# Performance work log

Measured on AMD Instinct MI355X. Metric: run time of the kernel, lower is better.

Reference implementation:

```python
import jax, jax.numpy as jnp
import numpy as np

N_NODES = 50000
N_EDGES = 640000
IN_CH = 128
OUT_CH = 128


def setup_inputs() -> dict:
    key = jax.random.key(0)
    k1, k2, k3, k4 = jax.random.split(key, 4)
    x = jax.random.normal(k1, (N_NODES, IN_CH), dtype=jnp.float32)
    edge_index = jax.random.randint(k2, (2, N_EDGES), 0, N_NODES, dtype=jnp.int32)
    # nn.Linear params: W [out, in], b [out]
    bound = 1.0 / np.sqrt(IN_CH)
    W = jax.random.uniform(k3, (OUT_CH, IN_CH), minval=-bound, maxval=bound, dtype=jnp.float32)
    b = jax.random.uniform(k4, (OUT_CH,), minval=-bound, maxval=bound, dtype=jnp.float32)
    return {"x": x, "edge_index": edge_index, "W": W, "b": b}


def reference(x, edge_index, W, b):
    row, col = edge_index[0], edge_index[1]
    num_nodes = x.shape[0]
    # degree of each destination node (clamped to >= 1)
    deg = jax.ops.segment_sum(jnp.ones(row.shape[0], dtype=x.dtype), row,
                              num_segments=num_nodes)
    deg = jnp.maximum(deg, 1.0)
    # gather neighbor features and scatter-add into destinations
    agg = jax.ops.segment_sum(x[col], row, num_segments=num_nodes)
    agg = agg / deg[:, None]
    # residual + linear
    return (x + agg) @ W.T + b
```

## Files before the change

kernel.cpp:

```cpp
#include <hip/hip_runtime.h>

#define N_NODES 50000
#define N_EDGES 640000
#define CH 128
#define NBINS 49
#define BINCAP 16384
#define CAPR 48
#define NTILES 782

typedef __bf16 bf16_t;
typedef bf16_t bf16x8 __attribute__((ext_vector_type(8)));
typedef float f32x4 __attribute__((ext_vector_type(4)));

__device__ __forceinline__ ushort f2bf(float f) {
  union { float f; unsigned u; } v; v.f = f;
  unsigned r = v.u + 0x7FFFu + ((v.u >> 16) & 1u);
  return (ushort)(r >> 16);
}
__device__ __forceinline__ float bflo(unsigned u) {
  union { unsigned u; float f; } v; v.u = u << 16; return v.f;
}
__device__ __forceinline__ float bfhi(unsigned u) {
  union { unsigned u; float f; } v; v.u = u & 0xFFFF0000u; return v.f;
}
__device__ __forceinline__ unsigned pack2(float lo, float hi) {
  return (unsigned)f2bf(lo) | ((unsigned)f2bf(hi) << 16);
}


__global__ __launch_bounds__(256) void init(const float4* __restrict__ W4,
                                            uint4* __restrict__ Wb4,
                                            int* __restrict__ bincur) {
  int i = blockIdx.x * 256 + threadIdx.x;
  if (i < NBINS) bincur[i] = 0;
  if (i < 2048) {
    float4 c = W4[i * 2], d = W4[i * 2 + 1];
    uint4 w;
    w.x = pack2(c.x, c.y); w.y = pack2(c.z, c.w);
    w.z = pack2(d.x, d.y); w.w = pack2(d.z, d.w);
    Wb4[i] = w;
  }
}

__global__ __launch_bounds__(256) void fill_conv(const int* __restrict__ row,
                                                 const int* __restrict__ col,
                                                 int* __restrict__ bincur,
                                                 unsigned* __restrict__ binArr,
                                                 const float4* __restrict__ x4,
                                                 uint4* __restrict__ xb4) {
  __shared__ int lh[NBINS];
  __shared__ int gbase[NBINS];
  int bid = blockIdx.x;
  int tid = threadIdx.x;
  if (bid < 625) {
    if (tid < NBINS) lh[tid] = 0;
    __syncthreads();
    int t = bid * 256 + tid;
    int4 r4 = *(const int4*)(row + t * 4);
    int4 c4 = *(const int4*)(col + t * 4);
    int rr[4] = {r4.x, r4.y, r4.z, r4.w};
    int cc[4] = {c4.x, c4.y, c4.z, c4.w};
    int bi[4], rk[4];
#pragma unroll
    for (int i = 0; i < 4; ++i) {
      bi[i] = rr[i] >> 10;
      rk[i] = atomicAdd(&lh[bi[i]], 1);
    }
    __syncthreads();
    if (tid < NBINS) {
      int c = lh[tid];
      gbase[tid] = (c > 0) ? atomicAdd(&bincur[tid], c) : 0;
    }
    __syncthreads();
#pragma unroll
    for (int i = 0; i < 4; ++i) {
      int pos = gbase[bi[i]] + rk[i];
      if (pos < BINCAP) {
        unsigned rec = ((unsigned)(rr[i] & 1023) << 16) | (unsigned)cc[i];
        binArr[bi[i] * BINCAP + pos] = rec;
      }
    }
  } else {
    int i = (bid - 625) * 256 + tid;
    float4 a = x4[i * 2], b = x4[i * 2 + 1];
    uint4 o;
    o.x = pack2(a.x, a.y); o.y = pack2(a.z, a.w);
    o.z = pack2(b.x, b.y); o.w = pack2(b.z, b.w);
    xb4[i] = o;
  }
}

__global__ __launch_bounds__(512) void fused(const uint4* __restrict__ xb4,
                                             const int* __restrict__ bincnt,
                                             const uint4* __restrict__ binArr4,
                                             const uint4* __restrict__ Wb4,
                                             const float4* __restrict__ bias4,
                                             float4* __restrict__ out4) {
  __shared__ ushort hT[64 * CH];
  __shared__ ushort colL[64 * CAPR];
  __shared__ int rowcnt[64];
  int tid = threadIdx.x;
  int g = blockIdx.x;
  int m0 = g * 64;

  if (tid < 64) rowcnt[tid] = 0;
  __syncthreads();
  {
    int b = g >> 4;
    int sub = g & 15;
    int bc = bincnt[b];
    const uint4* seg4 = binArr4 + b * (BINCAP / 4);
    for (int j = tid; j * 4 < bc; j += 512) {
      uint4 rv = seg4[j];
      int base = j * 4;
      unsigned recs[4] = {rv.x, rv.y, rv.z, rv.w};
#pragma unroll
      for (int i = 0; i < 4; ++i) {
        unsigned rec = recs[i];
        if (base + i < bc && (int)(rec >> 22) == sub) {
          int lr = (rec >> 16) & 63;
          int p = atomicAdd(&rowcnt[lr], 1);
          if (p < CAPR) colL[lr * CAPR + p] = (ushort)(rec & 0xFFFFu);
        }
      }
    }
  }
  __syncthreads();

  int wv = tid >> 6;
  int lane = tid & 63;
  int q = lane & 15;
  int grp = lane >> 4;
#pragma unroll
  for (int t = 0; t < 2; ++t) {
    int r = wv * 8 + t * 4 + grp;
    int node = m0 + r;
    int deg = rowcnt[r];
    int degc = deg < CAPR ? deg : CAPR;
    const ushort* arow = colL + r * CAPR;
    float acc[8] = {0.f, 0.f, 0.f, 0.f, 0.f, 0.f, 0.f, 0.f};
    int e = 0;
    for (; e + 3 < degc; e += 4) {
      uint2 ids = *(const uint2*)(arow + e);
      int n0 = ids.x & 0xFFFF, n1 = ids.x >> 16;
      int n2 = ids.y & 0xFFFF, n3 = ids.y >> 16;
      uint4 v0 = xb4[n0 * 16 + q];
      uint4 v1 = xb4[n1 * 16 + q];
      uint4 v2 = xb4[n2 * 16 + q];
      uint4 v3 = xb4[n3 * 16 + q];
      acc[0] += bflo(v0.x); acc[1] += bfhi(v0.x); acc[2] += bflo(v0.y); acc[3] += bfhi(v0.y);
      acc[4] += bflo(v0.z); acc[5] += bfhi(v0.z); acc[6] += bflo(v0.w); acc[7] += bfhi(v0.w);
      acc[0] += bflo(v1.x); acc[1] += bfhi(v1.x); acc[2] += bflo(v1.y); acc[3] += bfhi(v1.y);
      acc[4] += bflo(v1.z); acc[5] += bfhi(v1.z); acc[6] += bflo(v1.w); acc[7] += bfhi(v1.w);
      acc[0] += bflo(v2.x); acc[1] += bfhi(v2.x); acc[2] += bflo(v2.y); acc[3] += bfhi(v2.y);
      acc[4] += bflo(v2.z); acc[5] += bfhi(v2.z); acc[6] += bflo(v2.w); acc[7] += bfhi(v2.w);
      acc[0] += bflo(v3.x); acc[1] += bfhi(v3.x); acc[2] += bflo(v3.y); acc[3] += bfhi(v3.y);
      acc[4] += bflo(v3.z); acc[5] += bfhi(v3.z); acc[6] += bflo(v3.w); acc[7] += bfhi(v3.w);
    }
    for (; e < degc; ++e) {
      int nb = arow[e];
      uint4 v = xb4[nb * 16 + q];
      acc[0] += bflo(v.x); acc[1] += bfhi(v.x); acc[2] += bflo(v.y); acc[3] += bfhi(v.y);
      acc[4] += bflo(v.z); acc[5] += bfhi(v.z); acc[6] += bflo(v.w); acc[7] += bfhi(v.w);
    }
    uint4 o = make_uint4(0, 0, 0, 0);
    if (node < N_NODES) {
      float s = 1.0f / fmaxf((float)deg, 1.0f);
      uint4 xi = xb4[node * 16 + q];
      o.x = pack2(bflo(xi.x) + acc[0] * s, bfhi(xi.x) + acc[1] * s);
      o.y = pack2(bflo(xi.y) + acc[2] * s, bfhi(xi.y) + acc[3] * s);
      o.z = pack2(bflo(xi.z) + acc[4] * s, bfhi(xi.z) + acc[5] * s);
      o.w = pack2(bflo(xi.w) + acc[6] * s, bfhi(xi.w) + acc[7] * s);
    }
    *(uint4*)&hT[r * CH + q * 8] = o;
  }
  __syncthreads();

  int qq = grp;
  int mt = wv & 3;
  int nbase = (wv >> 2) * 4;
  const ushort* hrow = &hT[(mt * 16 + q) * CH + qq * 8];
  bf16x8 hb0 = *(const bf16x8*)(hrow);
  bf16x8 hb1 = *(const bf16x8*)(hrow + 32);
  bf16x8 hb2 = *(const bf16x8*)(hrow + 64);
  bf16x8 hb3 = *(const bf16x8*)(hrow + 96);
  int m = m0 + mt * 16 + q;
#pragma unroll
  for (int i = 0; i < 4; ++i) {
    int nt = nbase + i;
    const uint4* wr = Wb4 + (nt * 16 + q) * 16 + qq;
    bf16x8 w0 = __builtin_bit_cast(bf16x8, wr[0]);
    bf16x8 w1 = __builtin_bit_cast(bf16x8, wr[4]);
    bf16x8 w2 = __builtin_bit_cast(bf16x8, wr[8]);
    bf16x8 w3 = __builtin_bit_cast(bf16x8, wr[12]);
    f32x4 acc = {0.f, 0.f, 0.f, 0.f};
    acc = __builtin_amdgcn_mfma_f32_16x16x32_bf16(w0, hb0, acc, 0, 0, 0);
    acc = __builtin_amdgcn_mfma_f32_16x16x32_bf16(w1, hb1, acc, 0, 0, 0);
    acc = __builtin_amdgcn_mfma_f32_16x16x32_bf16(w2, hb2, acc, 0, 0, 0);
    acc = __builtin_amdgcn_mfma_f32_16x16x32_bf16(w3, hb3, acc, 0, 0, 0);
    if (m < N_NODES) {
      float4 bv = bias4[nt * 4 + qq];
      float4 o;
      o.x = acc[0] + bv.x;
      o.y = acc[1] + bv.y;
      o.z = acc[2] + bv.z;
      o.w = acc[3] + bv.w;
      out4[(size_t)m * 32 + nt * 4 + qq] = o;
    }
  }
}

extern "C" void kernel_launch(void* const* d_in, const int* in_sizes, int n_in,
                              void* d_out, int out_size, void* d_ws, size_t ws_size,
                              hipStream_t stream) {
  const float* x  = (const float*)d_in[0];
  const int*   ei = (const int*)d_in[1];
  const float* W  = (const float*)d_in[2];
  const float* bb = (const float*)d_in[3];

  char* ws = (char*)d_ws;
  int*      bincur = (int*)ws;
  unsigned* binArr = (unsigned*)(ws + 1024);
  uint4*    Wb4    = (uint4*)(ws + 3212288);
  uint4*    xb4    = (uint4*)(ws + 3245056);

  init<<<8, 256, 0, stream>>>((const float4*)W, Wb4, bincur);
  fill_conv<<<3750, 256, 0, stream>>>(ei, ei + N_EDGES, bincur, binArr,
                                      (const float4*)x, xb4);
  fused<<<NTILES, 512, 0, stream>>>(xb4, bincur, (const uint4*)binArr, Wb4,
                                    (const float4*)bb, (float4*)d_out);
}
```

Baseline: 138.1 us.

## Use finer 128-row edge bins, 32-row tiles, and fold W conversion into fill

Edges are now binned by groups of 128 destination rows (391 bins of 2048 capacity) instead of 1024, so each 32-row fused tile scans a 2048-slot bin rather than a 16384-slot one. This cuts the redundant bin scanning each block does to pick out its own rows. The fill kernel also processes 16 edges per thread, which reduces global atomics per block. The init kernel is replaced by a memset plus an extra fill block that converts W, and fused runs twice as many 256-thread blocks. The risks are bin overflow, since any edges beyond BINCAP are dropped, and more global atomics because there are more bins.

```diff
diff --git a/kernel.cpp b/kernel.cpp
--- a/kernel.cpp
+++ b/kernel.cpp
@@ -3,10 +3,11 @@
 #define N_NODES 50000
 #define N_EDGES 640000
 #define CH 128
-#define NBINS 49
-#define BINCAP 16384
+#define NBINS 391
+#define BINCAP 2048
 #define CAPR 48
-#define NTILES 782
+#define NTILES 1563
+#define FILLB 157
 
 typedef __bf16 bf16_t;
 typedef bf16_t bf16x8 __attribute__((ext_vector_type(8)));
@@ -27,98 +28,102 @@
   return (unsigned)f2bf(lo) | ((unsigned)f2bf(hi) << 16);
 }
 
-
-__global__ __launch_bounds__(256) void init(const float4* __restrict__ W4,
-                                            uint4* __restrict__ Wb4,
-                                            int* __restrict__ bincur) {
-  int i = blockIdx.x * 256 + threadIdx.x;
-  if (i < NBINS) bincur[i] = 0;
-  if (i < 2048) {
-    float4 c = W4[i * 2], d = W4[i * 2 + 1];
-    uint4 w;
-    w.x = pack2(c.x, c.y); w.y = pack2(c.z, c.w);
-    w.z = pack2(d.x, d.y); w.w = pack2(d.z, d.w);
-    Wb4[i] = w;
-  }
-}
 
 __global__ __launch_bounds__(256) void fill_conv(const int* __restrict__ row,
                                                  const int* __restrict__ col,
                                                  int* __restrict__ bincur,
                                                  unsigned* __restrict__ binArr,
                                                  const float4* __restrict__ x4,
-                                                 uint4* __restrict__ xb4) {
-  __shared__ int lh[NBINS];
-  __shared__ int gbase[NBINS];
+                                                 uint4* __restrict__ xb4,
+                                                 const float4* __restrict__ W4,
+                                                 uint4* __restrict__ Wb4) {
   int bid = blockIdx.x;
   int tid = threadIdx.x;
-  if (bid < 625) {
-    if (tid < NBINS) lh[tid] = 0;
+  if (bid < FILLB) {
+    __shared__ int lh[NBINS];
+    __shared__ int gb[NBINS];
+    for (int i = tid; i < NBINS; i += 256) lh[i] = 0;
     __syncthreads();
-    int t = bid * 256 + tid;
-    int4 r4 = *(const int4*)(row + t * 4);
-    int4 c4 = *(const int4*)(col + t * 4);
-    int rr[4] = {r4.x, r4.y, r4.z, r4.w};
-    int cc[4] = {c4.x, c4.y, c4.z, c4.w};
-    int bi[4], rk[4];
-#pragma unroll
-    for (int i = 0; i < 4; ++i) {
-      bi[i] = rr[i] >> 10;
-      rk[i] = atomicAdd(&lh[bi[i]], 1);
+    int base = bid * 4096 + tid * 16;
+    bool act = base < N_EDGES;
+    int rr[16], cc[16], bi[16], rk[16];
+    if (act) {
+#pragma unroll
+      for (int u = 0; u < 4; ++u) {
+        int4 r4 = *(const int4*)(row + base + u * 4);
+        int4 c4 = *(const int4*)(col + base + u * 4);
+        rr[u * 4 + 0] = r4.x; rr[u * 4 + 1] = r4.y; rr[u * 4 + 2] = r4.z; rr[u * 4 + 3] = r4.w;
+        cc[u * 4 + 0] = c4.x; cc[u * 4 + 1] = c4.y; cc[u * 4 + 2] = c4.z; cc[u * 4 + 3] = c4.w;
+      }
+#pragma unroll
+      for (int i = 0; i < 16; ++i) {
+        bi[i] = rr[i] >> 7;
+        rk[i] = atomicAdd(&lh[bi[i]], 1);
+      }
     }
     __syncthreads();
-    if (tid < NBINS) {
-      int c = lh[tid];
-      gbase[tid] = (c > 0) ? atomicAdd(&bincur[tid], c) : 0;
+    for (int i = tid; i < NBINS; i += 256) {
+      int c = lh[i];
+      gb[i] = c ? atomicAdd(&bincur[i], c) : 0;
     }
     __syncthreads();
-#pragma unroll
-    for (int i = 0; i < 4; ++i) {
-      int pos = gbase[bi[i]] + rk[i];
-      if (pos < BINCAP) {
-        unsigned rec = ((unsigned)(rr[i] & 1023) << 16) | (unsigned)cc[i];
-        binArr[bi[i] * BINCAP + pos] = rec;
-      }
-    }
-  } else {
-    int i = (bid - 625) * 256 + tid;
+    if (act) {
+#pragma unroll
+      for (int i = 0; i < 16; ++i) {
+        int pos = gb[bi[i]] + rk[i];
+        if (pos < BINCAP) {
+          binArr[bi[i] * BINCAP + pos] =
+              ((unsigned)(rr[i] & 127) << 16) | (unsigned)cc[i];
+        }
+      }
+    }
+  } else if (bid < FILLB + 3125) {
+    int i = (bid - FILLB) * 256 + tid;
     float4 a = x4[i * 2], b = x4[i * 2 + 1];
     uint4 o;
     o.x = pack2(a.x, a.y); o.y = pack2(a.z, a.w);
     o.z = pack2(b.x, b.y); o.w = pack2(b.z, b.w);
     xb4[i] = o;
-  }
-}
-
-__global__ __launch_bounds__(512) void fused(const uint4* __restrict__ xb4,
+  } else {
+    for (int i = tid; i < 2048; i += 256) {
+      float4 c = W4[i * 2], d = W4[i * 2 + 1];
+      uint4 w;
+      w.x = pack2(c.x, c.y); w.y = pack2(c.z, c.w);
+      w.z = pack2(d.x, d.y); w.w = pack2(d.z, d.w);
+      Wb4[i] = w;
+    }
+  }
+}
+
+__global__ __launch_bounds__(256) void fused(const uint4* __restrict__ xb4,
                                              const int* __restrict__ bincnt,
                                              const uint4* __restrict__ binArr4,
                                              const uint4* __restrict__ Wb4,
                                              const float4* __restrict__ bias4,
                                              float4* __restrict__ out4) {
-  __shared__ ushort hT[64 * CH];
-  __shared__ ushort colL[64 * CAPR];
-  __shared__ int rowcnt[64];
+  __shared__ ushort hT[32 * CH];
+  __shared__ ushort colL[32 * CAPR];
+  __shared__ int rowcnt[32];
   int tid = threadIdx.x;
   int g = blockIdx.x;
-  int m0 = g * 64;
-
-  if (tid < 64) rowcnt[tid] = 0;
+  int m0 = g * 32;
+
+  if (tid < 32) rowcnt[tid] = 0;
   __syncthreads();
   {
-    int b = g >> 4;
-    int sub = g & 15;
-    int bc = bincnt[b];
+    int b = g >> 2;
+    int sub = g & 3;
+    int bc = bincnt[b]; bc = bc < BINCAP ? bc : BINCAP;
     const uint4* seg4 = binArr4 + b * (BINCAP / 4);
-    for (int j = tid; j * 4 < bc; j += 512) {
+    for (int j = tid; j * 4 < bc; j += 256) {
       uint4 rv = seg4[j];
       int base = j * 4;
       unsigned recs[4] = {rv.x, rv.y, rv.z, rv.w};
 #pragma unroll
       for (int i = 0; i < 4; ++i) {
         unsigned rec = recs[i];
-        if (base + i < bc && (int)(rec >> 22) == sub) {
-          int lr = (rec >> 16) & 63;
+        if (base + i < bc && (int)((rec >> 21) & 3) == sub) {
+          int lr = (rec >> 16) & 31;
           int p = atomicAdd(&rowcnt[lr], 1);
           if (p < CAPR) colL[lr * CAPR + p] = (ushort)(rec & 0xFFFFu);
         }
@@ -177,8 +182,8 @@
   __syncthreads();
 
   int qq = grp;
-  int mt = wv & 3;
-  int nbase = (wv >> 2) * 4;
+  int mt = wv & 1;
+  int nbase = (wv >> 1) * 4;
   const ushort* hrow = &hT[(mt * 16 + q) * CH + qq * 8];
   bf16x8 hb0 = *(const bf16x8*)(hrow);
   bf16x8 hb1 = *(const bf16x8*)(hrow + 32);
@@ -220,13 +225,14 @@
 
   char* ws = (char*)d_ws;
   int*      bincur = (int*)ws;
-  unsigned* binArr = (unsigned*)(ws + 1024);
-  uint4*    Wb4    = (uint4*)(ws + 3212288);
-  uint4*    xb4    = (uint4*)(ws + 3245056);
-
-  init<<<8, 256, 0, stream>>>((const float4*)W, Wb4, bincur);
-  fill_conv<<<3750, 256, 0, stream>>>(ei, ei + N_EDGES, bincur, binArr,
-                                      (const float4*)x, xb4);
-  fused<<<NTILES, 512, 0, stream>>>(xb4, bincur, (const uint4*)binArr, Wb4,
+  unsigned* binArr = (unsigned*)(ws + 2048);
+  uint4*    Wb4    = (uint4*)(ws + 3205120);
+  uint4*    xb4    = (uint4*)(ws + 3237888);
+
+  hipMemsetAsync(bincur, 0, NBINS * sizeof(int), stream);
+  fill_conv<<<FILLB + 3125 + 1, 256, 0, stream>>>(ei, ei + N_EDGES, bincur,
+                                                  binArr, (const float4*)x, xb4,
+                                                  (const float4*)W, Wb4);
+  fused<<<NTILES, 256, 0, stream>>>(xb4, bincur, (const uint4*)binArr, Wb4,
                                     (const float4*)bb, (float4*)d_out);
 }
```

After: 128.2 us. 7.2% less time.
